# Optimization experiments

Measured on AMD Instinct MI355X. Metric: run time of the kernel, lower is better.

The kernel has to match this reference:

```python
import jax, jax.numpy as jnp
import numpy as np

NUM_HEADS = 12
HEAD_DIM = 64


def _rotate_half(x):
    x1, x2 = jnp.split(x, 2, axis=-1)
    return jnp.concatenate([-x2, x1], axis=-1)


def setup_inputs() -> dict:
    key = jax.random.key(0)
    ks = jax.random.split(key, 5)
    B, S, H = 4, 2048, 768
    x = jax.random.normal(ks[0], (B, S, H), dtype=jnp.float32)
    # rope tables per (batch, position, head_dim)
    pos = jnp.arange(S, dtype=jnp.float32)[:, None]
    inv = 1.0 / (10000.0 ** (jnp.arange(0, HEAD_DIM, 2, dtype=jnp.float32) / HEAD_DIM))
    ang = pos * inv[None, :]  # [S, hd/2]
    ang = jnp.concatenate([ang, ang], axis=-1)  # [S, hd]
    cos = jnp.broadcast_to(jnp.cos(ang)[None], (B, S, HEAD_DIM)).astype(jnp.float32)
    sin = jnp.broadcast_to(jnp.sin(ang)[None], (B, S, HEAD_DIM)).astype(jnp.float32)
    Wqkv = jax.random.normal(ks[1], (3 * H, H), dtype=jnp.float32) * 0.02
    Wo = jax.random.normal(ks[2], (H, H), dtype=jnp.float32) * 0.02
    return {"x": x, "cos": cos, "sin": sin, "Wqkv": Wqkv, "Wo": Wo, "window": 64}


def reference(x, cos, sin, Wqkv, Wo, window):
    B, S, H = x.shape
    nh, hd = NUM_HEADS, HEAD_DIM
    scale = hd ** -0.5
    qkv = jnp.einsum('bsh,oh->bso', x, Wqkv)  # [B,S,3H]
    qkv = qkv.reshape(B, S, 3, nh, hd)
    q = qkv[:, :, 0].transpose(0, 2, 1, 3)  # [B,nh,S,hd]
    k = qkv[:, :, 1].transpose(0, 2, 1, 3)
    v = qkv[:, :, 2].transpose(0, 2, 1, 3)
    # RoPE in float32, cos/sin broadcast over heads: [B,1,S,hd]
    c = cos[:, None].astype(jnp.float32)
    s = sin[:, None].astype(jnp.float32)
    qf, kf = q.astype(jnp.float32), k.astype(jnp.float32)
    q = (qf * c + _rotate_half(qf) * s).astype(q.dtype)
    k = (kf * c + _rotate_half(kf) * s).astype(k.dtype)
    scores = jnp.einsum('bhqd,bhkd->bhqk', q, k) * scale
    idx = jnp.arange(S)
    band = jnp.abs(idx[:, None] - idx[None, :]) <= window  # sliding-window mask
    scores = jnp.where(band[None, None], scores, -jnp.inf)
    probs = jax.nn.softmax(scores, axis=-1)
    y = jnp.einsum('bhqk,bhkd->bhqd', probs, v)  # [B,nh,S,hd]
    y = y.transpose(0, 2, 1, 3).reshape(B, S, H)
    return jnp.einsum('bsh,oh->bso', y, Wo)
```

## Files before the change

kernel.cpp:

```cpp
#include <hip/hip_runtime.h>


typedef __attribute__((ext_vector_type(8))) _Float16 f16x8;
typedef __attribute__((ext_vector_type(4))) float    f32x4;

#define BDIM 4
#define SDIM 2048
#define HDIM 768
#define NH   12
#define HD   64
#define NQKV 2304
#define MROWS 8192

#define MFMA16(a, b, c) __builtin_amdgcn_mfma_f32_16x16x32_f16(a, b, c, 0, 0, 0)

__device__ __forceinline__ void gload16(const void* g, void* l) {
    __builtin_amdgcn_global_load_lds(
        (__attribute__((address_space(1))) void*)(g),
        (__attribute__((address_space(3))) void*)(l),
        16, 0, 0);
}

__global__ __launch_bounds__(256) void cvt_all(
    const float* __restrict__ x,    _Float16* __restrict__ dx,
    const float* __restrict__ wqkv, _Float16* __restrict__ dq,
    const float* __restrict__ wo,   _Float16* __restrict__ dwo,
    const float* __restrict__ cosp, float* __restrict__ ctab,
    const float* __restrict__ sinp, float* __restrict__ stab)
{
    const int n0 = MROWS * HDIM / 8;
    const int n1 = NQKV * HDIM / 8;
    const int n2 = HDIM * HDIM / 8;
    const int n3 = SDIM * 32 / 8;
    int i = blockIdx.x * 256 + threadIdx.x;
    if (i >= n0 + n1 + n2) {
        int j = i - (n0 + n1 + n2);
        if (j >= n3) return;
        int s  = j >> 2;
        int i0 = (j & 3) << 3;
        const float4* cs = (const float4*)(cosp + (long)s * HD + i0);
        const float4* sn = (const float4*)(sinp + (long)s * HD + i0);
        float4* dc = (float4*)(ctab + s * 32 + i0);
        float4* dsn = (float4*)(stab + s * 32 + i0);
        dc[0] = cs[0];  dc[1] = cs[1];
        dsn[0] = sn[0]; dsn[1] = sn[1];
        return;
    }
    const float* s; _Float16* d; int j;
    if (i < n0)            { s = x;    d = dx;  j = i; }
    else if (i < n0 + n1)  { s = wqkv; d = dq;  j = i - n0; }
    else                   { s = wo;   d = dwo; j = i - n0 - n1; }
    const float4* s4 = (const float4*)s + (long)j * 2;
    float4 a = s4[0], b = s4[1];
    f16x8 o;
    o[0] = (_Float16)a.x; o[1] = (_Float16)a.y;
    o[2] = (_Float16)a.z; o[3] = (_Float16)a.w;
    o[4] = (_Float16)b.x; o[5] = (_Float16)b.y;
    o[6] = (_Float16)b.z; o[7] = (_Float16)b.w;
    *((f16x8*)d + j) = o;
}

__global__ __launch_bounds__(256) void gemm_qkv_t3(
    const _Float16* __restrict__ A,
    const _Float16* __restrict__ Bt,
    const float* __restrict__ ctab,
    const float* __restrict__ stab,
    _Float16* __restrict__ qh,
    _Float16* __restrict__ kh,
    _Float16* __restrict__ vh)
{
    const int K = HDIM;
    __shared__ __align__(16) _Float16 lsA[3][128 * 32];
    __shared__ __align__(16) _Float16 lsB[3][128 * 32];

    const int nTn = NQKV >> 7;
    int nwg = gridDim.x;
    int bid = blockIdx.x;
    int cpx = nwg >> 3;
    int wg  = (bid & 7) * cpx + (bid >> 3);
    int tm = wg / nTn, tn = wg % nTn;
    int m0 = tm << 7, n0 = tn << 7;

    int tid  = threadIdx.x;
    int lane = tid & 63;
    int w    = tid >> 6;
    int wr   = w >> 1, wc = w & 1;
    int l15  = lane & 15, lk = lane >> 4;

    f32x4 acc[4][4] = {};

    int srow = tid >> 2;
    int lg   = (tid & 3) ^ ((tid >> 3) & 3);
    const _Float16* gA = A  + (long)(m0 + srow) * K + lg * 8;
    const _Float16* gB = Bt + (long)(n0 + srow) * K + lg * 8;

    auto STAGE = [&](int buf, int t) {
        gload16(gA + t * 32,            &lsA[buf][tid * 8]);
        gload16(gA + t * 32 + 64L * K,  &lsA[buf][tid * 8 + 2048]);
        gload16(gB + t * 32,            &lsB[buf][tid * 8]);
        gload16(gB + t * 32 + 64L * K,  &lsB[buf][tid * 8 + 2048]);
    };
    auto RD = [&](const _Float16* base, int rbase, int f) -> f16x8 {
        int r = rbase + f * 16 + l15;
        int pg = lk ^ ((r >> 1) & 3);
        return *(const f16x8*)&base[r * 32 + pg * 8];
    };

    const int NT = K >> 5;

    STAGE(0, 0);
    STAGE(1, 1);
    asm volatile("s_waitcnt vmcnt(4)" ::: "memory");
    __builtin_amdgcn_s_barrier();

    int cur = 0;
    for (int t = 0; t < NT; ++t) {
        const _Float16* aC = lsA[cur];
        const _Float16* bC = lsB[cur];
        int stg = cur + 2; if (stg >= 3) stg -= 3;

        f16x8 af[4], bf[4];
#pragma unroll
        for (int mf = 0; mf < 4; ++mf) af[mf] = RD(aC, wr * 64, mf);
#pragma unroll
        for (int nf = 0; nf < 4; ++nf) bf[nf] = RD(bC, wc * 64, nf);
        if (t + 2 < NT) STAGE(stg, t + 2);

        __builtin_amdgcn_s_setprio(1);
#pragma unroll
        for (int mf = 0; mf < 4; ++mf)
#pragma unroll
            for (int nf = 0; nf < 4; ++nf)
                acc[mf][nf] = MFMA16(af[mf], bf[nf], acc[mf][nf]);
        __builtin_amdgcn_s_setprio(0);

        if (t + 1 < NT) {
            if (t + 2 < NT)
                asm volatile("s_waitcnt vmcnt(4)" ::: "memory");
            else
                asm volatile("s_waitcnt vmcnt(0)" ::: "memory");
            __builtin_amdgcn_s_barrier();
        }
        cur = cur + 1; if (cur == 3) cur = 0;
    }

    int ht = (n0 >> 6) + wc;
    int tq = ht / NH;
    int h  = ht - tq * NH;
    int b  = m0 >> 11;
    long base_bh = ((long)(b * NH + h)) * SDIM;
#pragma unroll
    for (int mf = 0; mf < 4; ++mf) {
#pragma unroll
        for (int j = 0; j < 4; ++j) {
            int gr = m0 + wr * 64 + mf * 16 + lk * 4 + j;
            int s  = gr & (SDIM - 1);
            if (tq == 2) {
#pragma unroll
                for (int nf = 0; nf < 4; ++nf) {
                    int d = nf * 16 + l15;
                    vh[(base_bh + s) * HD + d] = (_Float16)acc[mf][nf][j];
                }
            } else {
                float vals[4];
#pragma unroll
                for (int nf = 0; nf < 4; ++nf) vals[nf] = acc[mf][nf][j];
#pragma unroll
                for (int nf = 0; nf < 4; ++nf) {
                    int d  = nf * 16 + l15;
                    int di = ((nf & 1) << 4) + l15;
                    float cc = ctab[s * 32 + di];
                    float ss = stab[s * 32 + di];
                    float pv = (nf < 2) ? -vals[nf + 2] : vals[nf - 2];
                    float o  = vals[nf] * cc + pv * ss;
                    long oidx = (base_bh + s) * HD + d;
                    if (tq == 0) qh[oidx] = (_Float16)o;
                    else         kh[oidx] = (_Float16)o;
                }
            }
        }
    }
}

__global__ __launch_bounds__(256) void gemm_op8(
    const _Float16* __restrict__ A,
    const _Float16* __restrict__ Bt,
    float* __restrict__ C,
    int M, int N, int K)
{
    __shared__ __align__(16) _Float16 lsA[3][128 * 32];
    __shared__ __align__(16) _Float16 lsB[3][128 * 32];

    int nTn = N >> 7;
    int nwg = gridDim.x;
    int bid = blockIdx.x;
    int cpx = nwg >> 3;
    int wg  = (bid & 7) * cpx + (bid >> 3);
    int tm = wg / nTn, tn = wg % nTn;
    int m0 = tm << 7, n0 = tn << 7;

    int tid  = threadIdx.x;
    int lane = tid & 63;
    int w    = tid >> 6;
    int wr   = w >> 1, wc = w & 1;
    int l15  = lane & 15, lk = lane >> 4;

    f32x4 acc[4][4] = {};

    int srow = tid >> 2;
    int lg   = (tid & 3) ^ ((tid >> 3) & 3);
    const _Float16* gA = A  + (long)(m0 + srow) * K + lg * 8;
    const _Float16* gB = Bt + (long)(n0 + srow) * K + lg * 8;

    auto STAGE = [&](int buf, int t) {
        gload16(gA + t * 32,            &lsA[buf][tid * 8]);
        gload16(gA + t * 32 + 64L * K,  &lsA[buf][tid * 8 + 2048]);
        gload16(gB + t * 32,            &lsB[buf][tid * 8]);
        gload16(gB + t * 32 + 64L * K,  &lsB[buf][tid * 8 + 2048]);
    };
    auto RD = [&](const _Float16* base, int rbase, int f) -> f16x8 {
        int r = rbase + f * 16 + l15;
        int pg = lk ^ ((r >> 1) & 3);
        return *(const f16x8*)&base[r * 32 + pg * 8];
    };

    const int NT = K >> 5;

    STAGE(0, 0);
    STAGE(1, 1);
    asm volatile("s_waitcnt vmcnt(4)" ::: "memory");
    __builtin_amdgcn_s_barrier();

    int cur = 0;
    for (int t = 0; t < NT; ++t) {
        const _Float16* aC = lsA[cur];
        const _Float16* bC = lsB[cur];
        int stg = cur + 2; if (stg >= 3) stg -= 3;

        f16x8 af[4], bf[4];
#pragma unroll
        for (int mf = 0; mf < 4; ++mf) af[mf] = RD(aC, wr * 64, mf);
#pragma unroll
        for (int nf = 0; nf < 4; ++nf) bf[nf] = RD(bC, wc * 64, nf);
        if (t + 2 < NT) STAGE(stg, t + 2);

        __builtin_amdgcn_s_setprio(1);
#pragma unroll
        for (int mf = 0; mf < 4; ++mf)
#pragma unroll
            for (int nf = 0; nf < 4; ++nf)
                acc[mf][nf] = MFMA16(af[mf], bf[nf], acc[mf][nf]);
        __builtin_amdgcn_s_setprio(0);

        if (t + 1 < NT) {
            if (t + 2 < NT)
                asm volatile("s_waitcnt vmcnt(4)" ::: "memory");
            else
                asm volatile("s_waitcnt vmcnt(0)" ::: "memory");
            __builtin_amdgcn_s_barrier();
        }
        cur = cur + 1; if (cur == 3) cur = 0;
    }

#pragma unroll
    for (int mf = 0; mf < 4; ++mf)
#pragma unroll
        for (int nf = 0; nf < 4; ++nf)
#pragma unroll
            for (int j = 0; j < 4; ++j) {
                int gr = m0 + wr * 64 + mf * 16 + lk * 4 + j;
                int gc = n0 + wc * 64 + nf * 16 + l15;
                C[(long)gr * N + gc] = acc[mf][nf][j];
            }
}

#define SSTR 200
#define PSTR 200
__global__ __launch_bounds__(256) void attn_mfma(
    const _Float16* __restrict__ qh,
    const _Float16* __restrict__ kh,
    const _Float16* __restrict__ vh,
    _Float16* __restrict__ yh)
{
    __shared__ __align__(16) _Float16 lsVT[64 * SSTR];
    __shared__ __align__(16) _Float16 lsP [64 * PSTR];

    int bid = blockIdx.x;
    int qt  = bid & 31;
    int bh  = bid >> 5;
    int q0  = qt << 6;
    int k0  = q0 - 64;
    int tid = threadIdx.x;
    int lane = tid & 63;
    int w = tid >> 6;
    int l15 = lane & 15, lg = lane >> 4;

    const _Float16* Qb = qh + (long)bh * SDIM * HD;
    const _Float16* Kb = kh + (long)bh * SDIM * HD;
    const _Float16* Vb = vh + (long)bh * SDIM * HD;

#pragma unroll
    for (int c = 0; c < 3; ++c) {
        int rk = c * 64 + lane;
        int s  = k0 + rk;
        s = s < 0 ? 0 : (s >= SDIM ? SDIM - 1 : s);
        const f16x8* vr = (const f16x8*)(Vb + (long)s * HD + w * 16);
        f16x8 v0 = vr[0], v1 = vr[1];
#pragma unroll
        for (int e = 0; e < 8; ++e) {
            lsVT[(w * 16 + e)     * SSTR + rk] = v0[e];
            lsVT[(w * 16 + 8 + e) * SSTR + rk] = v1[e];
        }
    }

    int qrow = q0 + w * 16 + l15;
    const f16x8* qp = (const f16x8*)(Qb + (long)qrow * HD + lg * 8);
    f16x8 qa0 = qp[0];
    f16x8 qa1 = qp[4];

    float sums[4] = {0.f, 0.f, 0.f, 0.f};
    int iqb = w * 16 + lg * 4;
    int kt0 = w & ~1;
#pragma unroll 5
    for (int tt = 0; tt < 10; ++tt) {
        int kt = kt0 + tt;
        int krow = k0 + kt * 16 + l15;
        int kcl = krow < 0 ? 0 : (krow >= SDIM ? SDIM - 1 : krow);
        const f16x8* kp = (const f16x8*)(Kb + (long)kcl * HD + lg * 8);
        f16x8 kb0 = kp[0], kb1 = kp[4];
        f32x4 acc = {0.f, 0.f, 0.f, 0.f};
        acc = MFMA16(qa0, kb0, acc);
        acc = MFMA16(qa1, kb1, acc);
        int jk = kt * 16 + l15;
        bool kin = (krow >= 0) && (krow < SDIM);
#pragma unroll
        for (int j = 0; j < 4; ++j) {
            int i = iqb + j;
            bool valid = kin && (jk >= i) && (jk <= i + 128);
            float p = valid ? __expf(acc[j] * 0.125f) : 0.f;
            sums[j] += p;
            lsP[(w * 16 + lg * 4 + j) * PSTR + jk] = (_Float16)p;
        }
    }

#pragma unroll
    for (int m = 1; m < 16; m <<= 1) {
#pragma unroll
        for (int j = 0; j < 4; ++j)
            sums[j] += __shfl_xor(sums[j], m, 64);
    }
    float inv[4];
#pragma unroll
    for (int j = 0; j < 4; ++j) inv[j] = 1.f / sums[j];

    __syncthreads();

    f32x4 accy[4] = {};
    const _Float16* prow = &lsP[(w * 16 + l15) * PSTR + lg * 8];
    int kc0 = w >> 1;
#pragma unroll
    for (int c5 = 0; c5 < 5; ++c5) {
        int kc = kc0 + c5;
        f16x8 pa = *(const f16x8*)(prow + kc * 32);
#pragma unroll
        for (int dt = 0; dt < 4; ++dt) {
            f16x8 vb = *(const f16x8*)&lsVT[(dt * 16 + l15) * SSTR + kc * 32 + lg * 8];
            accy[dt] = MFMA16(pa, vb, accy[dt]);
        }
    }

    int b = bh / NH, h = bh - (bh / NH) * NH;
    long outbase = ((long)b * SDIM) * HDIM + (long)h * HD;
#pragma unroll
    for (int dt = 0; dt < 4; ++dt) {
#pragma unroll
        for (int j = 0; j < 4; ++j) {
            int srow = q0 + w * 16 + lg * 4 + j;
            yh[outbase + (long)srow * HDIM + dt * 16 + l15] =
                (_Float16)(accy[dt][j] * inv[j]);
        }
    }
}

extern "C" void kernel_launch(void* const* d_in, const int* in_sizes, int n_in,
                              void* d_out, int out_size, void* d_ws, size_t ws_size,
                              hipStream_t stream)
{
    const float* x    = (const float*)d_in[0];
    const float* cosp = (const float*)d_in[1];
    const float* sinp = (const float*)d_in[2];
    const float* Wqkv = (const float*)d_in[3];
    const float* Wo   = (const float*)d_in[4];
    float* out = (float*)d_out;

    char* ws = (char*)d_ws;
    _Float16* xh    = (_Float16*)(ws);
    _Float16* wqkvh = (_Float16*)(ws + 12582912);
    _Float16* woh   = (_Float16*)(ws + 16121856);
    _Float16* qh    = (_Float16*)(ws + 17301504);
    _Float16* kh    = (_Float16*)(ws + 29884416);
    _Float16* vh    = (_Float16*)(ws + 42467328);
    _Float16* yh    = (_Float16*)(ws + 55050240);
    float*    ctab  = (float*)   (ws + 67633152);
    float*    stab  = (float*)   (ws + 67895296);

    {
        int nthr = MROWS * HDIM / 8 + NQKV * HDIM / 8 + HDIM * HDIM / 8
                 + SDIM * 32 / 8;
        cvt_all<<<(nthr + 255) / 256, 256, 0, stream>>>(
            x, xh, Wqkv, wqkvh, Wo, woh, cosp, ctab, sinp, stab);
    }

    {
        dim3 grid((MROWS / 128) * (NQKV / 128));
        gemm_qkv_t3<<<grid, 256, 0, stream>>>(xh, wqkvh, ctab, stab, qh, kh, vh);
    }

    {
        dim3 grid(BDIM * NH * (SDIM / 64));
        attn_mfma<<<grid, 256, 0, stream>>>(qh, kh, vh, yh);
    }

    {
        dim3 grid((MROWS / 128) * (HDIM / 128));
        gemm_op8<<<grid, 256, 0, stream>>>(yh, woh, out, MROWS, HDIM, HDIM);
    }
}
```

Measured before the change: 101.2 us.

## Enlarge QKV GEMM tile to 256x128 with 512 threads and split-phase pipeline

Result: no change. 101.8 us (+0.6%).

```diff
diff --git a/kernel.cpp b/kernel.cpp
--- a/kernel.cpp
+++ b/kernel.cpp
@@ -60,7 +60,7 @@
     *((f16x8*)d + j) = o;
 }
 
-__global__ __launch_bounds__(256) void gemm_qkv_t3(
+__global__ __launch_bounds__(512) void gemm_qkv_p2(
     const _Float16* __restrict__ A,
     const _Float16* __restrict__ Bt,
     const float* __restrict__ ctab,
@@ -70,7 +70,7 @@
     _Float16* __restrict__ vh)
 {
     const int K = HDIM;
-    __shared__ __align__(16) _Float16 lsA[3][128 * 32];
+    __shared__ __align__(16) _Float16 lsA[3][256 * 32];
     __shared__ __align__(16) _Float16 lsB[3][128 * 32];
 
     const int nTn = NQKV >> 7;
@@ -79,7 +79,7 @@
     int cpx = nwg >> 3;
     int wg  = (bid & 7) * cpx + (bid >> 3);
     int tm = wg / nTn, tn = wg % nTn;
-    int m0 = tm << 7, n0 = tn << 7;
+    int m0 = tm << 8, n0 = tn << 7;
 
     int tid  = threadIdx.x;
     int lane = tid & 63;
@@ -94,12 +94,6 @@
     const _Float16* gA = A  + (long)(m0 + srow) * K + lg * 8;
     const _Float16* gB = Bt + (long)(n0 + srow) * K + lg * 8;
 
-    auto STAGE = [&](int buf, int t) {
-        gload16(gA + t * 32,            &lsA[buf][tid * 8]);
-        gload16(gA + t * 32 + 64L * K,  &lsA[buf][tid * 8 + 2048]);
-        gload16(gB + t * 32,            &lsB[buf][tid * 8]);
-        gload16(gB + t * 32 + 64L * K,  &lsB[buf][tid * 8 + 2048]);
-    };
     auto RD = [&](const _Float16* base, int rbase, int f) -> f16x8 {
         int r = rbase + f * 16 + l15;
         int pg = lk ^ ((r >> 1) & 3);
@@ -108,9 +102,15 @@
 
     const int NT = K >> 5;
 
-    STAGE(0, 0);
-    STAGE(1, 1);
-    asm volatile("s_waitcnt vmcnt(4)" ::: "memory");
+    {
+        gload16(gA,             &lsA[0][tid * 8]);
+        gload16(gA + 128L * K,  &lsA[0][tid * 8 + 4096]);
+        gload16(gB,             &lsB[0][tid * 8]);
+        gload16(gA + 32,            &lsA[1][tid * 8]);
+        gload16(gA + 32 + 128L * K, &lsA[1][tid * 8 + 4096]);
+        gload16(gB + 32,            &lsB[1][tid * 8]);
+    }
+    asm volatile("s_waitcnt vmcnt(3)" ::: "memory");
     __builtin_amdgcn_s_barrier();
 
     int cur = 0;
@@ -118,25 +118,44 @@
         const _Float16* aC = lsA[cur];
         const _Float16* bC = lsB[cur];
         int stg = cur + 2; if (stg >= 3) stg -= 3;
-
-        f16x8 af[4], bf[4];
+        bool pre = (t + 2 < NT);
+
+        f16x8 af[4], bf0, bf1;
 #pragma unroll
         for (int mf = 0; mf < 4; ++mf) af[mf] = RD(aC, wr * 64, mf);
-#pragma unroll
-        for (int nf = 0; nf < 4; ++nf) bf[nf] = RD(bC, wc * 64, nf);
-        if (t + 2 < NT) STAGE(stg, t + 2);
-
+        bf0 = RD(bC, wc * 64, 0);
+        bf1 = RD(bC, wc * 64, 1);
+        if (pre) {
+            gload16(gA + (t + 2) * 32,            &lsA[stg][tid * 8]);
+            gload16(gB + (t + 2) * 32,            &lsB[stg][tid * 8]);
+        }
+        __builtin_amdgcn_s_barrier();
         __builtin_amdgcn_s_setprio(1);
 #pragma unroll
-        for (int mf = 0; mf < 4; ++mf)
-#pragma unroll
-            for (int nf = 0; nf < 4; ++nf)
-                acc[mf][nf] = MFMA16(af[mf], bf[nf], acc[mf][nf]);
+        for (int mf = 0; mf < 4; ++mf) {
+            acc[mf][0] = MFMA16(af[mf], bf0, acc[mf][0]);
+            acc[mf][1] = MFMA16(af[mf], bf1, acc[mf][1]);
+        }
+        __builtin_amdgcn_s_setprio(0);
+        __builtin_amdgcn_s_barrier();
+
+        f16x8 bf2, bf3;
+        bf2 = RD(bC, wc * 64, 2);
+        bf3 = RD(bC, wc * 64, 3);
+        if (pre)
+            gload16(gA + (t + 2) * 32 + 128L * K, &lsA[stg][tid * 8 + 4096]);
+        __builtin_amdgcn_s_barrier();
+        __builtin_amdgcn_s_setprio(1);
+#pragma unroll
+        for (int mf = 0; mf < 4; ++mf) {
+            acc[mf][2] = MFMA16(af[mf], bf2, acc[mf][2]);
+            acc[mf][3] = MFMA16(af[mf], bf3, acc[mf][3]);
+        }
         __builtin_amdgcn_s_setprio(0);
 
         if (t + 1 < NT) {
             if (t + 2 < NT)
-                asm volatile("s_waitcnt vmcnt(4)" ::: "memory");
+                asm volatile("s_waitcnt vmcnt(3)" ::: "memory");
             else
                 asm volatile("s_waitcnt vmcnt(0)" ::: "memory");
             __builtin_amdgcn_s_barrier();
@@ -144,7 +163,7 @@
         cur = cur + 1; if (cur == 3) cur = 0;
     }
 
-    int ht = (n0 >> 6) + wc;
+    int ht = tn * 2 + wc;
     int tq = ht / NH;
     int h  = ht - tq * NH;
     int b  = m0 >> 11;
@@ -412,8 +431,8 @@
     }
 
     {
-        dim3 grid((MROWS / 128) * (NQKV / 128));
-        gemm_qkv_t3<<<grid, 256, 0, stream>>>(xh, wqkvh, ctab, stab, qh, kh, vh);
+        dim3 grid((MROWS / 256) * (NQKV / 128));
+        gemm_qkv_p2<<<grid, 512, 0, stream>>>(xh, wqkvh, ctab, stab, qh, kh, vh);
     }
 
     {
```
